# Kernel optimization log

Hardware: AMD Instinct MI355X
Metric: run time of the kernel (lower is better)

## Reference

```python
import jax, jax.numpy as jnp
import numpy as np

B, S, D, H, DIL = 4, 4096, 768, 12, 8
HD = D // H  # head dim = 64


def setup_inputs() -> dict:
    key = jax.random.key(0)
    ks = jax.random.split(key, 9)
    def w(k):
        return jax.random.normal(k, (D, D), jnp.float32) * 0.02
    def b(k):
        return jax.random.normal(k, (D,), jnp.float32) * 0.02
    return {
        "x": jax.random.normal(ks[0], (B, S, D), jnp.float32),
        "Wq": w(ks[1]), "bq": b(ks[2]),
        "Wk": w(ks[3]), "bk": b(ks[4]),
        "Wv": w(ks[5]), "bv": b(ks[6]),
        "Wo": w(ks[7]), "bo": b(ks[8]),
    }


def reference(x, Wq, bq, Wk, bk, Wv, bv, Wo, bo):
    Bs, Sl, _ = x.shape
    # torch.nn.Linear: y = x @ W.T + b
    q = (x @ Wq.T + bq).reshape(Bs, Sl, H, HD).transpose(0, 2, 1, 3)  # [B,H,S,hd]
    k = (x @ Wk.T + bk).reshape(Bs, Sl, H, HD).transpose(0, 2, 1, 3)
    v = (x @ Wv.T + bv).reshape(Bs, Sl, H, HD).transpose(0, 2, 1, 3)
    # Since S % DIL == 0, the per-position index set
    #   arange(max(0, i - DIL*(S//DIL)), min(S, i + DIL*(S//DIL)+1), DIL)
    # equals arange(0, S, DIL) for every i -> one batched gather + attention.
    idx = jnp.arange(0, Sl, DIL)
    k_d = k[:, :, idx, :]  # [B,H,S/DIL,hd]
    v_d = v[:, :, idx, :]
    scale = 1.0 / np.sqrt(HD).astype(np.float32)
    scores = jnp.einsum('bhqd,bhkd->bhqk', q, k_d) * scale  # [B,H,S,S/DIL]
    attn = jax.nn.softmax(scores, axis=-1)  # dropout: eval mode, identity
    ctx = jnp.einsum('bhqk,bhkd->bhqd', attn, v_d)  # [B,H,S,hd]
    ctx = ctx.transpose(0, 2, 1, 3).reshape(Bs, Sl, D)
    return ctx @ Wo.T + bo
```

## Files before the change

### kernel.cpp

```cpp
#include <hip/hip_runtime.h>

typedef __attribute__((ext_vector_type(8))) short short8;
typedef __attribute__((ext_vector_type(4))) short short4v;
typedef __attribute__((ext_vector_type(4))) float f32x4;

#define AS1 __attribute__((address_space(1)))
#define AS3 __attribute__((address_space(3)))

__device__ __forceinline__ void gld16(const void* g, void* l) {
  __builtin_amdgcn_global_load_lds((const AS1 void*)g, (AS3 void*)l, 16, 0, 0);
}

__device__ __forceinline__ short f2bf(float f) {
  unsigned u = __builtin_bit_cast(unsigned, f);
  unsigned r = (u + 0x7fffu + ((u >> 16) & 1u)) >> 16;
  return (short)r;
}

#define MFMA(a, b, c) __builtin_amdgcn_mfma_f32_16x16x32_bf16((a), (b), (c), 0, 0, 0)

__global__ void cast_f32_bf16(const float* __restrict__ in, short* __restrict__ out, int n4) {
  int i = blockIdx.x * 256 + threadIdx.x;
  if (i >= n4) return;
  f32x4 v = ((const f32x4*)in)[i];
  short4v o;
  o[0] = f2bf(v[0]); o[1] = f2bf(v[1]); o[2] = f2bf(v[2]); o[3] = f2bf(v[3]);
  ((short4v*)out)[i] = o;
}

template <int OUT>
__global__ __launch_bounds__(256) void gemm_bt(const short* __restrict__ A, int lda,
                                               const short* __restrict__ B,
                                               const float* __restrict__ bias,
                                               void* __restrict__ Cv, int K,
                                               float oscale) {
  __shared__ alignas(16) short As[128 * 32];
  __shared__ alignas(16) short Bs[128 * 32];
  const int tid = threadIdx.x, wave = tid >> 6, lane = tid & 63;
  const int bm = blockIdx.x * 128, bn = blockIdx.y * 128;
  const int wr = (wave >> 1) * 64, wc = (wave & 1) * 64;
  const int l15 = lane & 15, g = lane >> 4;
  const int srow = lane >> 2;
  const int skoff = (lane & 3) * 8;

  f32x4 zero = {0.f, 0.f, 0.f, 0.f};
  f32x4 acc[4][4];
#pragma unroll
  for (int m = 0; m < 4; ++m)
#pragma unroll
    for (int n = 0; n < 4; ++n) acc[m][n] = zero;

  for (int kt = 0; kt < K; kt += 32) {
#pragma unroll
    for (int c = 0; c < 2; ++c) {
      int chunk = wave * 2 + c;
      int r = chunk * 16 + srow;
      gld16(A + (size_t)(bm + r) * lda + kt + skoff, (char*)As + chunk * 1024);
      gld16(B + (size_t)(bn + r) * 768 + kt + skoff, (char*)Bs + chunk * 1024);
    }
    __syncthreads();
    short8 af[4], bfr[4];
#pragma unroll
    for (int m = 0; m < 4; ++m)
      af[m] = *(const short8*)((const char*)As + (wr + 16 * m + l15) * 64 + g * 16);
#pragma unroll
    for (int n = 0; n < 4; ++n)
      bfr[n] = *(const short8*)((const char*)Bs + (wc + 16 * n + l15) * 64 + g * 16);
#pragma unroll
    for (int m = 0; m < 4; ++m)
#pragma unroll
      for (int n = 0; n < 4; ++n) acc[m][n] = MFMA(af[m], bfr[n], acc[m][n]);
    __syncthreads();
  }

#pragma unroll
  for (int m = 0; m < 4; ++m)
#pragma unroll
    for (int n = 0; n < 4; ++n) {
      int col = bn + wc + 16 * n + l15;
      float bv = bias[col];
      if (OUT == 2) {
        int row0 = bm + wr + 16 * m + g * 4;
        short4v pk;
#pragma unroll
        for (int r = 0; r < 4; ++r) pk[r] = f2bf((acc[m][n][r] + bv) * oscale);
        size_t addr = (size_t)((row0 >> 9) * 12 + (col >> 6)) * 32768 +
                      (size_t)(col & 63) * 512 + (row0 & 511);
        *(short4v*)((short*)Cv + addr) = pk;
      } else {
#pragma unroll
        for (int r = 0; r < 4; ++r) {
          int row = bm + wr + 16 * m + g * 4 + r;
          float v = (acc[m][n][r] + bv) * oscale;
          if (OUT == 1)
            ((short*)Cv)[(size_t)row * 768 + col] = f2bf(v);
          else
            ((float*)Cv)[(size_t)row * 768 + col] = v;
        }
      }
    }
}

__global__ __launch_bounds__(256) void attn_kernel(const short* __restrict__ qb,
                                                   const short* __restrict__ kb,
                                                   const short* __restrict__ vt,
                                                   short* __restrict__ ctxb) {
  __shared__ alignas(16) char kv[32768];
  __shared__ alignas(16) char plds[4096];
  const int tid = threadIdx.x, wave = tid >> 6, lane = tid & 63;
  const int b = blockIdx.y / 12, h = blockIdx.y % 12;
  const int qbase = blockIdx.x * 64;
  const int l15 = lane & 15, g = lane >> 4;

  const short* qrow = qb + (size_t)(b * 4096 + qbase + wave * 16 + l15) * 768 + h * 64 + g * 8;
  short8 qa0 = *(const short8*)(qrow);
  short8 qa1 = *(const short8*)(qrow + 32);

  float s_[128];
  f32x4 zero = {0.f, 0.f, 0.f, 0.f};

#pragma unroll
  for (int hh = 0; hh < 2; ++hh) {
#pragma unroll
    for (int c = 0; c < 8; ++c) {
      int chunk = wave * 8 + c;
      int key = chunk * 8 + (lane >> 3);
      int sb = ((lane & 7) * 16) ^ ((key & 7) << 4);
      gld16(kb + (size_t)(b * 512 + hh * 256 + key) * 768 + h * 64 + (sb >> 1),
            kv + chunk * 1024);
    }
    __syncthreads();
#pragma unroll
    for (int t = 0; t < 16; ++t) {
      int base = (t * 16 + l15) * 128;
      int swz = (lane & 7) << 4;
      short8 k0 = *(const short8*)(kv + ((base + g * 16) ^ swz));
      short8 k1 = *(const short8*)(kv + ((base + 64 + g * 16) ^ swz));
      f32x4 a = MFMA(qa0, k0, zero);
      a = MFMA(qa1, k1, a);
#pragma unroll
      for (int r = 0; r < 4; ++r) s_[(hh * 16 + t) * 4 + r] = a[r];
    }
    __syncthreads();
  }

  float mrow[4] = {-1e30f, -1e30f, -1e30f, -1e30f};
#pragma unroll
  for (int t = 0; t < 32; ++t)
#pragma unroll
    for (int r = 0; r < 4; ++r) mrow[r] = fmaxf(mrow[r], s_[t * 4 + r]);
#pragma unroll
  for (int r = 0; r < 4; ++r) {
    mrow[r] = fmaxf(mrow[r], __shfl_xor(mrow[r], 1, 64));
    mrow[r] = fmaxf(mrow[r], __shfl_xor(mrow[r], 2, 64));
    mrow[r] = fmaxf(mrow[r], __shfl_xor(mrow[r], 4, 64));
    mrow[r] = fmaxf(mrow[r], __shfl_xor(mrow[r], 8, 64));
  }
  float rsum[4] = {0.f, 0.f, 0.f, 0.f};
#pragma unroll
  for (int t = 0; t < 32; ++t)
#pragma unroll
    for (int r = 0; r < 4; ++r) {
      float p = __builtin_amdgcn_exp2f(s_[t * 4 + r] - mrow[r]);
      s_[t * 4 + r] = p;
      rsum[r] += p;
    }
#pragma unroll
  for (int r = 0; r < 4; ++r) {
    rsum[r] += __shfl_xor(rsum[r], 1, 64);
    rsum[r] += __shfl_xor(rsum[r], 2, 64);
    rsum[r] += __shfl_xor(rsum[r], 4, 64);
    rsum[r] += __shfl_xor(rsum[r], 8, 64);
  }
  float rinv[4];
#pragma unroll
  for (int r = 0; r < 4; ++r) rinv[r] = 1.0f / rsum[r];

  f32x4 ctx[4];
#pragma unroll
  for (int n = 0; n < 4; ++n) ctx[n] = zero;
  char* pw = plds + wave * 1024;

#pragma unroll
  for (int vv = 0; vv < 2; ++vv) {
#pragma unroll
    for (int c = 0; c < 8; ++c) {
      int chunk = wave * 8 + c;
      int d = chunk * 2 + (lane >> 5);
      int sb = ((lane & 31) * 16) ^ ((d & 7) << 4);
      gld16(vt + (size_t)((b * 12 + h) * 64 + d) * 512 + vv * 256 + (sb >> 1),
            kv + chunk * 1024);
    }
    __syncthreads();
#pragma unroll
    for (int kk = 0; kk < 8; ++kk) {
#pragma unroll
      for (int tt = 0; tt < 2; ++tt)
#pragma unroll
        for (int r = 0; r < 4; ++r) {
          int row = g * 4 + r;
          int byte = (row * 64 + (tt * 16 + l15) * 2) ^ ((row & 7) << 4);
          *(short*)(pw + byte) = f2bf(s_[(vv * 16 + kk * 2 + tt) * 4 + r]);
        }
      short8 pa = *(const short8*)(pw + ((l15 * 64 + g * 16) ^ ((lane & 7) << 4)));
#pragma unroll
      for (int n = 0; n < 4; ++n) {
        int row = 16 * n + l15;
        int byte = (row * 512 + kk * 64 + g * 16) ^ ((row & 7) << 4);
        short8 vf = *(const short8*)(kv + byte);
        ctx[n] = MFMA(pa, vf, ctx[n]);
      }
    }
    __syncthreads();
  }

  size_t rowbase = (size_t)(b * 4096 + qbase + wave * 16);
#pragma unroll
  for (int n = 0; n < 4; ++n)
#pragma unroll
    for (int r = 0; r < 4; ++r) {
      int row = g * 4 + r;
      float v = ctx[n][r] * rinv[r];
      ctxb[(rowbase + row) * 768 + h * 64 + 16 * n + l15] = f2bf(v);
    }
}

extern "C" void kernel_launch(void* const* d_in, const int* in_sizes, int n_in,
                              void* d_out, int out_size, void* d_ws, size_t ws_size,
                              hipStream_t stream) {
  const float* x  = (const float*)d_in[0];
  const float* Wq = (const float*)d_in[1];
  const float* bq = (const float*)d_in[2];
  const float* Wk = (const float*)d_in[3];
  const float* bk = (const float*)d_in[4];
  const float* Wv = (const float*)d_in[5];
  const float* bv = (const float*)d_in[6];
  const float* Wo = (const float*)d_in[7];
  const float* bo = (const float*)d_in[8];

  char* ws = (char*)d_ws;
  const size_t XB_OFF = 0;
  const size_t WQ_OFF = 25165824;
  const size_t WK_OFF = WQ_OFF + 1179648;
  const size_t WV_OFF = WK_OFF + 1179648;
  const size_t WO_OFF = WV_OFF + 1179648;
  const size_t Q_OFF  = WO_OFF + 1179648;
  const size_t K_OFF  = Q_OFF + 25165824;
  const size_t V_OFF  = K_OFF + 3145728;

  short* xb   = (short*)(ws + XB_OFF);
  short* ctxb = xb;
  short* wqb  = (short*)(ws + WQ_OFF);
  short* wkb  = (short*)(ws + WK_OFF);
  short* wvb  = (short*)(ws + WV_OFF);
  short* wob  = (short*)(ws + WO_OFF);
  short* qbf  = (short*)(ws + Q_OFF);
  short* kbf  = (short*)(ws + K_OFF);
  short* vtb  = (short*)(ws + V_OFF);

  cast_f32_bf16<<<12288, 256, 0, stream>>>(x, xb, 3145728);
  cast_f32_bf16<<<576, 256, 0, stream>>>(Wq, wqb, 147456);
  cast_f32_bf16<<<576, 256, 0, stream>>>(Wk, wkb, 147456);
  cast_f32_bf16<<<576, 256, 0, stream>>>(Wv, wvb, 147456);
  cast_f32_bf16<<<576, 256, 0, stream>>>(Wo, wob, 147456);

  const float QSCALE = 0.18033688011112042f;

  gemm_bt<1><<<dim3(128, 6), 256, 0, stream>>>(xb, 768, wqb, bq, qbf, 768, QSCALE);
  gemm_bt<1><<<dim3(16, 6), 256, 0, stream>>>(xb, 6144, wkb, bk, kbf, 768, 1.0f);
  gemm_bt<2><<<dim3(16, 6), 256, 0, stream>>>(xb, 6144, wvb, bv, vtb, 768, 1.0f);

  attn_kernel<<<dim3(64, 48), 256, 0, stream>>>(qbf, kbf, vtb, ctxb);

  gemm_bt<0><<<dim3(128, 6), 256, 0, stream>>>(ctxb, 768, wob, bo, d_out, 768, 1.0f);
}
```

Before: 281.9 us.

## Double-buffer attention K/V staging, keep P in registers, fuse K/V projections

The attention kernel is rebuilt around a two-buffer LDS pipeline. It stages K and V in 128-key chunks with explicit vmcnt waits and barriers, so the loads overlap the MFMA work. QK^T is computed transposed, which lets the softmax probabilities feed PV straight from registers instead of going through LDS. V^T is written in a permuted key order that matches the register layout of P. The four weight casts are merged into one launch, and the K and V projection GEMMs are fused into one launch with 2x columns. The price is more register pressure (launch bounds 2, 32 f32x4 scores per lane) and fragile hand-written waitcnt ordering.

Measured after the change: 245.4 us. 13.0% less time.

```diff
diff --git a/kernel.cpp b/kernel.cpp
--- a/kernel.cpp
+++ b/kernel.cpp
@@ -16,6 +16,12 @@
   unsigned r = (u + 0x7fffu + ((u >> 16) & 1u)) >> 16;
   return (short)r;
 }
+
+template <int N>
+__device__ __forceinline__ void wait_vm() {
+  asm volatile("s_waitcnt vmcnt(%0)" ::"i"(N) : "memory");
+}
+__device__ __forceinline__ void bar() { __builtin_amdgcn_s_barrier(); }
 
 #define MFMA(a, b, c) __builtin_amdgcn_mfma_f32_16x16x32_bf16((a), (b), (c), 0, 0, 0)
 
@@ -28,12 +34,24 @@
   ((short4v*)out)[i] = o;
 }
 
+__global__ void cast4_f32_bf16(const float* __restrict__ s0, const float* __restrict__ s1,
+                               const float* __restrict__ s2, const float* __restrict__ s3,
+                               short* __restrict__ out) {
+  const float* src = (blockIdx.y == 0) ? s0 : (blockIdx.y == 1) ? s1 : (blockIdx.y == 2) ? s2 : s3;
+  int i = blockIdx.x * 256 + threadIdx.x;
+  f32x4 v = ((const f32x4*)src)[i];
+  short4v o;
+  o[0] = f2bf(v[0]); o[1] = f2bf(v[1]); o[2] = f2bf(v[2]); o[3] = f2bf(v[3]);
+  ((short4v*)(out + (size_t)blockIdx.y * 589824))[i] = o;
+}
+
 template <int OUT>
 __global__ __launch_bounds__(256) void gemm_bt(const short* __restrict__ A, int lda,
                                                const short* __restrict__ B,
                                                const float* __restrict__ bias,
-                                               void* __restrict__ Cv, int K,
-                                               float oscale) {
+                                               const float* __restrict__ bias2,
+                                               void* __restrict__ Cv, void* __restrict__ Cv2,
+                                               int K, float oscale) {
   __shared__ alignas(16) short As[128 * 32];
   __shared__ alignas(16) short Bs[128 * 32];
   const int tid = threadIdx.x, wave = tid >> 6, lane = tid & 63;
@@ -78,151 +96,176 @@
 #pragma unroll
     for (int n = 0; n < 4; ++n) {
       int col = bn + wc + 16 * n + l15;
-      float bv = bias[col];
-      if (OUT == 2) {
+      if (OUT == 3 && col >= 768) {
+        float bv = bias2[col - 768];
+        int hh = col - 768;
+        int h = hh >> 6, d = hh & 63;
         int row0 = bm + wr + 16 * m + g * 4;
+        int bb = row0 >> 9, kloc = row0 & 511;
+        int slot = ((kloc >> 5) << 5) + (((kloc >> 2) & 3) << 3) + (((kloc >> 4) & 1) << 2);
         short4v pk;
 #pragma unroll
         for (int r = 0; r < 4; ++r) pk[r] = f2bf((acc[m][n][r] + bv) * oscale);
-        size_t addr = (size_t)((row0 >> 9) * 12 + (col >> 6)) * 32768 +
-                      (size_t)(col & 63) * 512 + (row0 & 511);
-        *(short4v*)((short*)Cv + addr) = pk;
+        *(short4v*)((short*)Cv2 + (size_t)((bb * 12 + h) * 64 + d) * 512 + slot) = pk;
       } else {
+        float bv = bias[col];
 #pragma unroll
         for (int r = 0; r < 4; ++r) {
           int row = bm + wr + 16 * m + g * 4 + r;
           float v = (acc[m][n][r] + bv) * oscale;
-          if (OUT == 1)
+          if (OUT == 0)
+            ((float*)Cv)[(size_t)row * 768 + col] = v;
+          else
             ((short*)Cv)[(size_t)row * 768 + col] = f2bf(v);
-          else
-            ((float*)Cv)[(size_t)row * 768 + col] = v;
         }
       }
     }
 }
 
-__global__ __launch_bounds__(256) void attn_kernel(const short* __restrict__ qb,
-                                                   const short* __restrict__ kb,
-                                                   const short* __restrict__ vt,
-                                                   short* __restrict__ ctxb) {
-  __shared__ alignas(16) char kv[32768];
-  __shared__ alignas(16) char plds[4096];
+__global__ __launch_bounds__(256, 2) void attn_kernel(const short* __restrict__ qb,
+                                                      const short* __restrict__ kb,
+                                                      const short* __restrict__ vt,
+                                                      short* __restrict__ ctxb) {
+  __shared__ alignas(16) char lds[32768];
+  char* bufA = lds;
+  char* bufB = lds + 16384;
   const int tid = threadIdx.x, wave = tid >> 6, lane = tid & 63;
   const int b = blockIdx.y / 12, h = blockIdx.y % 12;
   const int qbase = blockIdx.x * 64;
-  const int l15 = lane & 15, g = lane >> 4;
+  const int l15 = lane & 15, g = lane >> 4, g4 = g * 4;
 
   const short* qrow = qb + (size_t)(b * 4096 + qbase + wave * 16 + l15) * 768 + h * 64 + g * 8;
   short8 qa0 = *(const short8*)(qrow);
   short8 qa1 = *(const short8*)(qrow + 32);
 
-  float s_[128];
   f32x4 zero = {0.f, 0.f, 0.f, 0.f};
-
-#pragma unroll
-  for (int hh = 0; hh < 2; ++hh) {
-#pragma unroll
-    for (int c = 0; c < 8; ++c) {
-      int chunk = wave * 8 + c;
-      int key = chunk * 8 + (lane >> 3);
-      int sb = ((lane & 7) * 16) ^ ((key & 7) << 4);
-      gld16(kb + (size_t)(b * 512 + hh * 256 + key) * 768 + h * 64 + (sb >> 1),
-            kv + chunk * 1024);
+  f32x4 st[32];
+
+  const int krow_g = (lane & 7) * 16;
+  const int kkey = wave * 32 + (lane >> 3);
+  const int vd = wave * 16 + (lane >> 4);
+  const int vcol = (lane & 15) * 16;
+  const size_t kgbase = (size_t)(b * 512) * 768 + h * 64;
+  const size_t vgbase = (size_t)((b * 12 + h) * 64) * 512;
+  const int kswz = (l15 & 7) << 4;
+
+#define STAGE_K(ci, dst)                                                              \
+  _Pragma("unroll") for (int c = 0; c < 4; ++c) {                                     \
+    int key = kkey + c * 8;                                                           \
+    int sb = krow_g ^ ((key & 7) << 4);                                               \
+    gld16(kb + kgbase + (size_t)((ci)*128 + key) * 768 + (sb >> 1),                   \
+          (dst) + (wave * 32 + c * 8) * 128);                                         \
+  }
+#define STAGE_V(ci, dst)                                                              \
+  _Pragma("unroll") for (int c = 0; c < 4; ++c) {                                     \
+    int d = vd + c * 4;                                                               \
+    int sb = vcol ^ ((d & 7) << 4);                                                   \
+    gld16(vt + vgbase + (size_t)d * 512 + (ci)*128 + (sb >> 1),                       \
+          (dst) + (wave * 16 + c * 4) * 256);                                         \
+  }
+#define QK_CHUNK(ci, buf)                                                             \
+  __builtin_amdgcn_s_setprio(1);                                                      \
+  _Pragma("unroll") for (int t = 0; t < 8; ++t) {                                     \
+    int base = (t * 16 + l15) * 128;                                                  \
+    short8 k0 = *(const short8*)((buf) + (base + ((g * 16) ^ kswz)));                 \
+    short8 k1 = *(const short8*)((buf) + (base + ((g * 16 + 64) ^ kswz)));            \
+    f32x4 a = MFMA(k0, qa0, zero);                                                    \
+    st[(ci)*8 + t] = MFMA(k1, qa1, a);                                                \
+  }                                                                                   \
+  __builtin_amdgcn_s_setprio(0);
+#define PV_CHUNK(ci, buf)                                                             \
+  __builtin_amdgcn_s_setprio(1);                                                      \
+  _Pragma("unroll") for (int kk = 0; kk < 4; ++kk) {                                  \
+    f32x4 s0 = st[(ci)*8 + 2 * kk], s1 = st[(ci)*8 + 2 * kk + 1];                     \
+    short8 pa;                                                                        \
+    pa[0] = f2bf(s0[0]); pa[1] = f2bf(s0[1]); pa[2] = f2bf(s0[2]); pa[3] = f2bf(s0[3]);\
+    pa[4] = f2bf(s1[0]); pa[5] = f2bf(s1[1]); pa[6] = f2bf(s1[2]); pa[7] = f2bf(s1[3]);\
+    _Pragma("unroll") for (int n = 0; n < 4; ++n) {                                   \
+      int row = 16 * n + l15;                                                         \
+      short8 vf = *(const short8*)((buf) + row * 256 + ((kk * 64 + g * 16) ^ ((row & 7) << 4))); \
+      ctx[n] = MFMA(pa, vf, ctx[n]);                                                  \
+    }                                                                                 \
+  }                                                                                   \
+  __builtin_amdgcn_s_setprio(0);
+
+  STAGE_K(0, bufA);
+  STAGE_K(1, bufB);
+
+  wait_vm<4>(); bar();
+  QK_CHUNK(0, bufA);
+  bar(); asm volatile("" ::: "memory");
+  STAGE_K(2, bufA);
+
+  wait_vm<4>(); bar();
+  QK_CHUNK(1, bufB);
+  bar(); asm volatile("" ::: "memory");
+  STAGE_K(3, bufB);
+
+  wait_vm<4>(); bar();
+  QK_CHUNK(2, bufA);
+  bar(); asm volatile("" ::: "memory");
+  STAGE_V(0, bufA);
+
+  wait_vm<4>(); bar();
+  QK_CHUNK(3, bufB);
+  bar(); asm volatile("" ::: "memory");
+  STAGE_V(1, bufB);
+
+  float m = st[0][0];
+#pragma unroll
+  for (int t = 0; t < 32; ++t)
+#pragma unroll
+    for (int r = 0; r < 4; ++r) m = fmaxf(m, st[t][r]);
+  m = fmaxf(m, __shfl_xor(m, 16, 64));
+  m = fmaxf(m, __shfl_xor(m, 32, 64));
+  float l = 0.f;
+#pragma unroll
+  for (int t = 0; t < 32; ++t)
+#pragma unroll
+    for (int r = 0; r < 4; ++r) {
+      float p = __builtin_amdgcn_exp2f(st[t][r] - m);
+      st[t][r] = p;
+      l += p;
     }
-    __syncthreads();
-#pragma unroll
-    for (int t = 0; t < 16; ++t) {
-      int base = (t * 16 + l15) * 128;
-      int swz = (lane & 7) << 4;
-      short8 k0 = *(const short8*)(kv + ((base + g * 16) ^ swz));
-      short8 k1 = *(const short8*)(kv + ((base + 64 + g * 16) ^ swz));
-      f32x4 a = MFMA(qa0, k0, zero);
-      a = MFMA(qa1, k1, a);
-#pragma unroll
-      for (int r = 0; r < 4; ++r) s_[(hh * 16 + t) * 4 + r] = a[r];
-    }
-    __syncthreads();
+  l += __shfl_xor(l, 16, 64);
+  l += __shfl_xor(l, 32, 64);
+
+  f32x4 ctx[4];
+#pragma unroll
+  for (int n = 0; n < 4; ++n) ctx[n] = zero;
+
+  wait_vm<4>(); bar();
+  PV_CHUNK(0, bufA);
+  bar(); asm volatile("" ::: "memory");
+  STAGE_V(2, bufA);
+
+  wait_vm<4>(); bar();
+  PV_CHUNK(1, bufB);
+  bar(); asm volatile("" ::: "memory");
+  STAGE_V(3, bufB);
+
+  wait_vm<4>(); bar();
+  PV_CHUNK(2, bufA);
+
+  wait_vm<0>(); bar();
+  PV_CHUNK(3, bufB);
+
+  float rinv = 1.0f / l;
+  float rw0 = __shfl(rinv, g4, 64), rw1 = __shfl(rinv, g4 + 1, 64);
+  float rw2 = __shfl(rinv, g4 + 2, 64), rw3 = __shfl(rinv, g4 + 3, 64);
+  size_t rowbase = (size_t)(b * 4096 + qbase + wave * 16);
+#pragma unroll
+  for (int n = 0; n < 4; ++n) {
+    int col = h * 64 + 16 * n + l15;
+    ctxb[(rowbase + g4 + 0) * 768 + col] = f2bf(ctx[n][0] * rw0);
+    ctxb[(rowbase + g4 + 1) * 768 + col] = f2bf(ctx[n][1] * rw1);
+    ctxb[(rowbase + g4 + 2) * 768 + col] = f2bf(ctx[n][2] * rw2);
+    ctxb[(rowbase + g4 + 3) * 768 + col] = f2bf(ctx[n][3] * rw3);
   }
-
-  float mrow[4] = {-1e30f, -1e30f, -1e30f, -1e30f};
-#pragma unroll
-  for (int t = 0; t < 32; ++t)
-#pragma unroll
-    for (int r = 0; r < 4; ++r) mrow[r] = fmaxf(mrow[r], s_[t * 4 + r]);
-#pragma unroll
-  for (int r = 0; r < 4; ++r) {
-    mrow[r] = fmaxf(mrow[r], __shfl_xor(mrow[r], 1, 64));
-    mrow[r] = fmaxf(mrow[r], __shfl_xor(mrow[r], 2, 64));
-    mrow[r] = fmaxf(mrow[r], __shfl_xor(mrow[r], 4, 64));
-    mrow[r] = fmaxf(mrow[r], __shfl_xor(mrow[r], 8, 64));
-  }
-  float rsum[4] = {0.f, 0.f, 0.f, 0.f};
-#pragma unroll
-  for (int t = 0; t < 32; ++t)
-#pragma unroll
-    for (int r = 0; r < 4; ++r) {
-      float p = __builtin_amdgcn_exp2f(s_[t * 4 + r] - mrow[r]);
-      s_[t * 4 + r] = p;
-      rsum[r] += p;
-    }
-#pragma unroll
-  for (int r = 0; r < 4; ++r) {
-    rsum[r] += __shfl_xor(rsum[r], 1, 64);
-    rsum[r] += __shfl_xor(rsum[r], 2, 64);
-    rsum[r] += __shfl_xor(rsum[r], 4, 64);
-    rsum[r] += __shfl_xor(rsum[r], 8, 64);
-  }
-  float rinv[4];
-#pragma unroll
-  for (int r = 0; r < 4; ++r) rinv[r] = 1.0f / rsum[r];
-
-  f32x4 ctx[4];
-#pragma unroll
-  for (int n = 0; n < 4; ++n) ctx[n] = zero;
-  char* pw = plds + wave * 1024;
-
-#pragma unroll
-  for (int vv = 0; vv < 2; ++vv) {
-#pragma unroll
-    for (int c = 0; c < 8; ++c) {
-      int chunk = wave * 8 + c;
-      int d = chunk * 2 + (lane >> 5);
-      int sb = ((lane & 31) * 16) ^ ((d & 7) << 4);
-      gld16(vt + (size_t)((b * 12 + h) * 64 + d) * 512 + vv * 256 + (sb >> 1),
-            kv + chunk * 1024);
-    }
-    __syncthreads();
-#pragma unroll
-    for (int kk = 0; kk < 8; ++kk) {
-#pragma unroll
-      for (int tt = 0; tt < 2; ++tt)
-#pragma unroll
-        for (int r = 0; r < 4; ++r) {
-          int row = g * 4 + r;
-          int byte = (row * 64 + (tt * 16 + l15) * 2) ^ ((row & 7) << 4);
-          *(short*)(pw + byte) = f2bf(s_[(vv * 16 + kk * 2 + tt) * 4 + r]);
-        }
-      short8 pa = *(const short8*)(pw + ((l15 * 64 + g * 16) ^ ((lane & 7) << 4)));
-#pragma unroll
-      for (int n = 0; n < 4; ++n) {
-        int row = 16 * n + l15;
-        int byte = (row * 512 + kk * 64 + g * 16) ^ ((row & 7) << 4);
-        short8 vf = *(const short8*)(kv + byte);
-        ctx[n] = MFMA(pa, vf, ctx[n]);
-      }
-    }
-    __syncthreads();
-  }
-
-  size_t rowbase = (size_t)(b * 4096 + qbase + wave * 16);
-#pragma unroll
-  for (int n = 0; n < 4; ++n)
-#pragma unroll
-    for (int r = 0; r < 4; ++r) {
-      int row = g * 4 + r;
-      float v = ctx[n][r] * rinv[r];
-      ctxb[(rowbase + row) * 768 + h * 64 + 16 * n + l15] = f2bf(v);
-    }
+#undef STAGE_K
+#undef STAGE_V
+#undef QK_CHUNK
+#undef PV_CHUNK
 }
 
 extern "C" void kernel_launch(void* const* d_in, const int* in_sizes, int n_in,
@@ -252,25 +295,20 @@
   short* ctxb = xb;
   short* wqb  = (short*)(ws + WQ_OFF);
   short* wkb  = (short*)(ws + WK_OFF);
-  short* wvb  = (short*)(ws + WV_OFF);
   short* wob  = (short*)(ws + WO_OFF);
   short* qbf  = (short*)(ws + Q_OFF);
   short* kbf  = (short*)(ws + K_OFF);
   short* vtb  = (short*)(ws + V_OFF);
 
   cast_f32_bf16<<<12288, 256, 0, stream>>>(x, xb, 3145728);
-  cast_f32_bf16<<<576, 256, 0, stream>>>(Wq, wqb, 147456);
-  cast_f32_bf16<<<576, 256, 0, stream>>>(Wk, wkb, 147456);
-  cast_f32_bf16<<<576, 256, 0, stream>>>(Wv, wvb, 147456);
-  cast_f32_bf16<<<576, 256, 0, stream>>>(Wo, wob, 147456);
+  cast4_f32_bf16<<<dim3(576, 4), 256, 0, stream>>>(Wq, Wk, Wv, Wo, wqb);
 
   const float QSCALE = 0.18033688011112042f;
 
-  gemm_bt<1><<<dim3(128, 6), 256, 0, stream>>>(xb, 768, wqb, bq, qbf, 768, QSCALE);
-  gemm_bt<1><<<dim3(16, 6), 256, 0, stream>>>(xb, 6144, wkb, bk, kbf, 768, 1.0f);
-  gemm_bt<2><<<dim3(16, 6), 256, 0, stream>>>(xb, 6144, wvb, bv, vtb, 768, 1.0f);
+  gemm_bt<1><<<dim3(128, 6), 256, 0, stream>>>(xb, 768, wqb, bq, nullptr, qbf, nullptr, 768, QSCALE);
+  gemm_bt<3><<<dim3(16, 12), 256, 0, stream>>>(xb, 6144, wkb, bk, bv, kbf, vtb, 768, 1.0f);
 
   attn_kernel<<<dim3(64, 48), 256, 0, stream>>>(qbf, kbf, vtb, ctxb);
 
-  gemm_bt<0><<<dim3(128, 6), 256, 0, stream>>>(ctxb, 768, wob, bo, d_out, 768, 1.0f);
-}
+  gemm_bt<0><<<dim3(128, 6), 256, 0, stream>>>(ctxb, 768, wob, bo, nullptr, d_out, nullptr, 768, 1.0f);
+}
```
